# Optimization experiments

Hardware: AMD Instinct MI355X
Metric: run time of the kernel (lower is better)

Reference implementation:

```python
import jax, jax.numpy as jnp
import numpy as np

N_NODES = 100000
N_EDGES = 3200000
IN_DIM = 512
HID_DIM = 16


def spmm(edge_src, edge_dst, edge_weight, feats):
    # out[i] = sum_{(j->i) in E} w_e * feats[j]  (sparse adj @ feats)
    gathered = feats[edge_src] * edge_weight[:, None]  # [E, D]
    return jax.ops.segment_sum(gathered, edge_dst, num_segments=N_NODES)


def setup_inputs() -> dict:
    key = jax.random.key(0)
    ks = jax.random.split(key, 8)
    x = jax.random.normal(ks[0], (N_NODES, IN_DIM), dtype=jnp.float32)
    edge_src = jax.random.randint(ks[1], (N_EDGES,), 0, N_NODES, dtype=jnp.int32)
    edge_dst = jax.random.randint(ks[2], (N_EDGES,), 0, N_NODES, dtype=jnp.int32)
    # normalized adjacency weights (positive, small, like D^-1/2 A D^-1/2 entries)
    edge_weight = jax.random.uniform(ks[3], (N_EDGES,), dtype=jnp.float32) * 0.1
    # Glorot-style init for GraphConvolution weights
    W1 = jax.random.normal(ks[4], (IN_DIM, HID_DIM), dtype=jnp.float32) * (1.0 / np.sqrt(IN_DIM))
    b1 = jnp.zeros((HID_DIM,), dtype=jnp.float32)
    W2 = jax.random.normal(ks[5], (HID_DIM, 1), dtype=jnp.float32) * (1.0 / np.sqrt(HID_DIM))
    b2 = jnp.zeros((1,), dtype=jnp.float32)
    return {"x": x, "edge_src": edge_src, "edge_dst": edge_dst,
            "edge_weight": edge_weight, "W1": W1, "b1": b1, "W2": W2, "b2": b2}


def reference(x, edge_src, edge_dst, edge_weight, W1, b1, W2, b2):
    # Layer 1: GraphConvolution(input_dim -> hidden_dim) + ReLU
    h = spmm(edge_src, edge_dst, edge_weight, x @ W1) + b1  # [N, 16]
    h = jax.nn.relu(h)
    # dropout is identity in eval mode (training=False)
    # Layer 2: GraphConvolution(hidden_dim -> 1)
    out = spmm(edge_src, edge_dst, edge_weight, h @ W2) + b2  # [N, 1]
    return out
```

## Files before the change

kernel.cpp:

```cpp
#include <hip/hip_runtime.h>
#include <hip/hip_fp16.h>

#define N_NODES 100000
#define N_EDGES 3200000
#define IN_DIM  512
#define HID_DIM 16

#define B_BKT   782
#define BKT_SH  7
#define EPB     12500
#define CAP_MAX 4608

#define G1_TILES 6250

typedef __attribute__((ext_vector_type(8))) short bf16x8;
typedef __attribute__((ext_vector_type(4))) float f32x4;

__device__ __forceinline__ void atomic_add_f32(float* p, float v) {
    __hip_atomic_fetch_add(p, v, __ATOMIC_RELAXED, __HIP_MEMORY_SCOPE_AGENT);
}
__device__ __forceinline__ int atomic_add_i32(int* p, int v) {
    return __hip_atomic_fetch_add(p, v, __ATOMIC_RELAXED, __HIP_MEMORY_SCOPE_AGENT);
}

__device__ __forceinline__ unsigned short bf16_rne(float f) {
    unsigned u = __float_as_uint(f);
    return (unsigned short)((u + 0x7fffu + ((u >> 16) & 1u)) >> 16);
}

__global__ void z0_init(int* __restrict__ cursor, int cap) {
    int b = blockIdx.x * blockDim.x + threadIdx.x;
    if (b < B_BKT) cursor[b] = b * cap;
}

__global__ __launch_bounds__(256) void g1_xw_mfma(const float* __restrict__ x,
                                                  const float* __restrict__ W1,
                                                  __half* __restrict__ xwh) {
    __shared__ alignas(16) unsigned short whi[16 * 64 * 8];
    __shared__ alignas(16) unsigned short wlo[16 * 64 * 8];
    const int t = threadIdx.x;

    for (int idx = t; idx < 16 * 64 * 8; idx += 256) {
        int c  = idx >> 9;
        int l  = (idx >> 3) & 63;
        int tt = idx & 7;
        int k  = c * 32 + ((l >> 4) << 3) + tt;
        int j  = l & 15;
        float w = W1[k * HID_DIM + j];
        unsigned u = __float_as_uint(w);
        float hif = __uint_as_float(u & 0xffff0000u);
        whi[idx] = (unsigned short)(u >> 16);
        wlo[idx] = bf16_rne(w - hif);
    }
    __syncthreads();

    const int lane = t & 63;
    const int wid  = blockIdx.x * 4 + (t >> 6);
    if (wid >= G1_TILES) return;
    const int row0 = wid * 16;

    const float* xrow = x + (size_t)(row0 + (lane & 15)) * IN_DIM + ((lane >> 4) << 3);
    const unsigned short* whp = &whi[lane * 8];
    const unsigned short* wlp = &wlo[lane * 8];

    f32x4 acc = {0.f, 0.f, 0.f, 0.f};
    float4 a0 = *(const float4*)(xrow);
    float4 a1 = *(const float4*)(xrow + 4);
#pragma unroll
    for (int c = 0; c < 16; ++c) {
        float4 n0, n1;
        if (c < 15) {
            n0 = *(const float4*)(xrow + (c + 1) * 32);
            n1 = *(const float4*)(xrow + (c + 1) * 32 + 4);
        }
        float av[8] = {a0.x, a0.y, a0.z, a0.w, a1.x, a1.y, a1.z, a1.w};
        bf16x8 ah, al;
#pragma unroll
        for (int e = 0; e < 8; ++e) {
            unsigned u = __float_as_uint(av[e]);
            ah[e] = (short)(u >> 16);
            float lof = av[e] - __uint_as_float(u & 0xffff0000u);
            al[e] = (short)bf16_rne(lof);
        }
        bf16x8 bh = *(const bf16x8*)(whp + (size_t)c * 512);
        bf16x8 bl = *(const bf16x8*)(wlp + (size_t)c * 512);
        acc = __builtin_amdgcn_mfma_f32_16x16x32_bf16(ah, bh, acc, 0, 0, 0);
        acc = __builtin_amdgcn_mfma_f32_16x16x32_bf16(al, bh, acc, 0, 0, 0);
        acc = __builtin_amdgcn_mfma_f32_16x16x32_bf16(ah, bl, acc, 0, 0, 0);
        a0 = n0; a1 = n1;
    }

    const int n     = lane & 15;
    const int rbase = row0 + ((lane >> 4) << 2);
#pragma unroll
    for (int i = 0; i < 4; ++i)
        xwh[(size_t)(rbase + i) * HID_DIM + n] = __float2half_rn(acc[i]);
}

__global__ __launch_bounds__(1024) void s1_bin(const int* __restrict__ src,
                                               const int* __restrict__ dst,
                                               const float* __restrict__ wgt,
                                               int* __restrict__ cursor,
                                               uint2* __restrict__ rec, int cap) {
    __shared__ int hist[B_BKT];
    __shared__ int base[B_BKT];
    const int t = threadIdx.x;
    for (int b = t; b < B_BKT; b += 1024) hist[b] = 0;
    __syncthreads();
    const int e0 = blockIdx.x * EPB;
    const int4*   d4 = (const int4*)(dst + e0);
    const int4*   s4 = (const int4*)(src + e0);
    const float4* w4 = (const float4*)(wgt + e0);
    const int NG = EPB / 4;
    for (int g = t; g < NG; g += 1024) {
        int4 d = d4[g];
        atomicAdd(&hist[d.x >> BKT_SH], 1);
        atomicAdd(&hist[d.y >> BKT_SH], 1);
        atomicAdd(&hist[d.z >> BKT_SH], 1);
        atomicAdd(&hist[d.w >> BKT_SH], 1);
    }
    __syncthreads();
    for (int b = t; b < B_BKT; b += 1024) {
        int c = hist[b];
        base[b] = c > 0 ? atomic_add_i32(&cursor[b], c) : 0;
    }
    __syncthreads();
    for (int b = t; b < B_BKT; b += 1024) hist[b] = 0;
    __syncthreads();
    for (int g = t; g < NG; g += 1024) {
        int4 d = d4[g];
        int4 s = s4[g];
        float4 w = w4[g];
        {
            int b = d.x >> BKT_SH;
            int pos = base[b] + atomicAdd(&hist[b], 1);
            rec[pos] = make_uint2(((unsigned)s.x << BKT_SH) | (unsigned)(d.x & 127),
                                  __float_as_uint(w.x));
        }
        {
            int b = d.y >> BKT_SH;
            int pos = base[b] + atomicAdd(&hist[b], 1);
            rec[pos] = make_uint2(((unsigned)s.y << BKT_SH) | (unsigned)(d.y & 127),
                                  __float_as_uint(w.y));
        }
        {
            int b = d.z >> BKT_SH;
            int pos = base[b] + atomicAdd(&hist[b], 1);
            rec[pos] = make_uint2(((unsigned)s.z << BKT_SH) | (unsigned)(d.z & 127),
                                  __float_as_uint(w.z));
        }
        {
            int b = d.w >> BKT_SH;
            int pos = base[b] + atomicAdd(&hist[b], 1);
            rec[pos] = make_uint2(((unsigned)s.w << BKT_SH) | (unsigned)(d.w & 127),
                                  __float_as_uint(w.w));
        }
    }
}

__global__ __launch_bounds__(512) void s2_sort(const int* __restrict__ cursor,
                                               uint2* __restrict__ rec,
                                               int2* __restrict__ row, int cap) {
    __shared__ uint2 srec[CAP_MAX];
    __shared__ int ocnt[128], scn[128], cur[128];
    const int t = threadIdx.x;
    const int bkt = blockIdx.x;
    const int e0 = bkt * cap;
    int n = cursor[bkt] - e0;
    n = max(0, min(n, cap));
    if (t < 128) ocnt[t] = 0;
    __syncthreads();
    for (int i = t; i < n; i += 512) {
        uint2 r = rec[e0 + i];
        srec[i] = r;
        atomicAdd(&ocnt[r.x & 127u], 1);
    }
    __syncthreads();
    if (t < 128) scn[t] = ocnt[t];
    __syncthreads();
    for (int off = 1; off < 128; off <<= 1) {
        int v = 0;
        if (t < 128 && t >= off) v = scn[t - off];
        __syncthreads();
        if (t < 128 && t >= off) scn[t] += v;
        __syncthreads();
    }
    if (t < 128) {
        int b = scn[t] - ocnt[t];
        cur[t] = b;
        int node = (bkt << BKT_SH) + t;
        if (node < N_NODES) row[node] = make_int2(e0 + b, ocnt[t]);
    }
    __syncthreads();
    for (int i = t; i < n; i += 512) {
        uint2 r = srec[i];
        int d = (int)(r.x & 127u);
        int pos = atomicAdd(&cur[d], 1);
        rec[e0 + pos] = make_uint2(r.x >> BKT_SH, r.y);
    }
}

__global__ __launch_bounds__(256) void p4_layer1(const int2* __restrict__ row,
                                                 const uint2* __restrict__ rec,
                                                 const __half* __restrict__ xwh,
                                                 const float* __restrict__ b1,
                                                 const float* __restrict__ W2,
                                                 float* __restrict__ hw) {
    const int t = threadIdx.x;
    const int node = blockIdx.x * 16 + (t >> 4);
    const int j = t & 15;
    int2 r = row[node];
    int e = r.x;
    const int end = r.x + r.y;
    float acc = 0.0f;
    for (; e + 4 <= end; e += 4) {
        uint2 q0 = rec[e], q1 = rec[e + 1], q2 = rec[e + 2], q3 = rec[e + 3];
        float f0 = __half2float(xwh[(size_t)q0.x * HID_DIM + j]);
        float f1 = __half2float(xwh[(size_t)q1.x * HID_DIM + j]);
        float f2 = __half2float(xwh[(size_t)q2.x * HID_DIM + j]);
        float f3 = __half2float(xwh[(size_t)q3.x * HID_DIM + j]);
        acc += __uint_as_float(q0.y) * f0;
        acc += __uint_as_float(q1.y) * f1;
        acc += __uint_as_float(q2.y) * f2;
        acc += __uint_as_float(q3.y) * f3;
    }
    for (; e < end; ++e) {
        uint2 q = rec[e];
        acc += __uint_as_float(q.y) * __half2float(xwh[(size_t)q.x * HID_DIM + j]);
    }
    float v = fmaxf(acc + b1[j], 0.0f) * W2[j];
    v += __shfl_xor(v, 1);
    v += __shfl_xor(v, 2);
    v += __shfl_xor(v, 4);
    v += __shfl_xor(v, 8);
    if (j == 0) hw[node] = v;
}

__global__ __launch_bounds__(256) void p5_layer2(const int2* __restrict__ row,
                                                 const uint2* __restrict__ rec,
                                                 const float* __restrict__ hwv,
                                                 const float* __restrict__ b2,
                                                 float* __restrict__ out) {
    const int t = threadIdx.x;
    const int node = blockIdx.x * 32 + (t >> 3);
    const int i = t & 7;
    int2 r = row[node];
    const int end = r.x + r.y;
    int k = r.x + i;
    float s = 0.0f;
    for (; k + 24 < end; k += 32) {
        uint2 a = rec[k], b = rec[k + 8], c = rec[k + 16], d = rec[k + 24];
        float ha = hwv[a.x], hb = hwv[b.x], hc = hwv[c.x], hd = hwv[d.x];
        s += __uint_as_float(a.y) * ha + __uint_as_float(b.y) * hb
           + __uint_as_float(c.y) * hc + __uint_as_float(d.y) * hd;
    }
    for (; k < end; k += 8) {
        uint2 a = rec[k];
        s += __uint_as_float(a.y) * hwv[a.x];
    }
    s += __shfl_xor(s, 1);
    s += __shfl_xor(s, 2);
    s += __shfl_xor(s, 4);
    if (i == 0) out[node] = b2[0] + s;
}

__global__ void f0_zero(float* __restrict__ h, const float* __restrict__ b2,
                        float* __restrict__ out) {
    int i = blockIdx.x * blockDim.x + threadIdx.x;
    if (i < N_NODES * HID_DIM) h[i] = 0.0f;
    if (i < N_NODES) out[i] = b2[0];
}
__global__ void k2_spmm1(const int* __restrict__ src, const int* __restrict__ dst,
                         const float* __restrict__ wgt, const __half* __restrict__ xwh,
                         float* __restrict__ h) {
    int t = blockIdx.x * blockDim.x + threadIdx.x;
    int e = t >> 4;
    int j = t & (HID_DIM - 1);
    if (e < N_EDGES) {
        float v = wgt[e] * __half2float(xwh[(size_t)src[e] * HID_DIM + j]);
        atomic_add_f32(&h[(size_t)dst[e] * HID_DIM + j], v);
    }
}
__global__ void k3_act(const float* __restrict__ h, const float* __restrict__ b1,
                       const float* __restrict__ W2, float* __restrict__ hw) {
    int i = blockIdx.x * blockDim.x + threadIdx.x;
    if (i >= N_NODES) return;
    const float4* h4 = (const float4*)(h + (size_t)i * HID_DIM);
    const float4* b4 = (const float4*)b1;
    const float4* w4 = (const float4*)W2;
    float acc = 0.0f;
#pragma unroll
    for (int q = 0; q < HID_DIM / 4; ++q) {
        float4 hv = h4[q]; float4 bv = b4[q]; float4 wv = w4[q];
        acc += fmaxf(hv.x + bv.x, 0.0f) * wv.x;
        acc += fmaxf(hv.y + bv.y, 0.0f) * wv.y;
        acc += fmaxf(hv.z + bv.z, 0.0f) * wv.z;
        acc += fmaxf(hv.w + bv.w, 0.0f) * wv.w;
    }
    hw[i] = acc;
}
__global__ void k4_spmm2(const int* __restrict__ src, const int* __restrict__ dst,
                         const float* __restrict__ wgt, const float* __restrict__ hw,
                         float* __restrict__ out) {
    int e = blockIdx.x * blockDim.x + threadIdx.x;
    if (e < N_EDGES) atomic_add_f32(&out[dst[e]], wgt[e] * hw[src[e]]);
}


extern "C" void kernel_launch(void* const* d_in, const int* in_sizes, int n_in,
                              void* d_out, int out_size, void* d_ws, size_t ws_size,
                              hipStream_t stream) {
    const float* x    = (const float*)d_in[0];
    const int*   esrc = (const int*)  d_in[1];
    const int*   edst = (const int*)  d_in[2];
    const float* ew   = (const float*)d_in[3];
    const float* W1   = (const float*)d_in[4];
    const float* b1   = (const float*)d_in[5];
    const float* W2   = (const float*)d_in[6];
    const float* b2   = (const float*)d_in[7];
    float* out = (float*)d_out;
    char* ws = (char*)d_ws;

    __half* xwh    = (__half*)ws;
    float*  hw     = (float*)(ws + (size_t)N_NODES * HID_DIM * 2);
    int*    cursor = (int*)(hw + N_NODES);
    int2*   row    = (int2*)(((size_t)(cursor + B_BKT) + 7) & ~(size_t)7);
    size_t rec_off = ((size_t)((char*)(row + N_NODES) - ws) + 15) & ~(size_t)15;
    uint2* rec = (uint2*)(ws + rec_off);

    int cap = 0;
    if (ws_size > rec_off) {
        size_t cap_fit = (ws_size - rec_off) / ((size_t)B_BKT * sizeof(uint2));
        cap = (int)(cap_fit < CAP_MAX ? cap_fit : CAP_MAX);
    }

    if (cap >= 4480) {
        z0_init<<<(B_BKT + 255) / 256, 256, 0, stream>>>(cursor, cap);
        g1_xw_mfma<<<(G1_TILES + 3) / 4, 256, 0, stream>>>(x, W1, xwh);
        s1_bin<<<N_EDGES / EPB, 1024, 0, stream>>>(esrc, edst, ew, cursor, rec, cap);
        s2_sort<<<B_BKT, 512, 0, stream>>>(cursor, rec, row, cap);
        p4_layer1<<<N_NODES / 16, 256, 0, stream>>>(row, rec, xwh, b1, W2, hw);
        p5_layer2<<<N_NODES / 32, 256, 0, stream>>>(row, rec, hw, b2, out);
    } else {
        __half* f_xwh = (__half*)ws;
        float*  f_h   = (float*)(ws + (size_t)N_NODES * HID_DIM * 2);
        float*  f_hw  = f_h + (size_t)N_NODES * HID_DIM;
        int n = N_NODES * HID_DIM;
        f0_zero<<<(n + 255) / 256, 256, 0, stream>>>(f_h, b2, out);
        g1_xw_mfma<<<(G1_TILES + 3) / 4, 256, 0, stream>>>(x, W1, f_xwh);
        k2_spmm1<<<(N_EDGES * 16) / 256, 256, 0, stream>>>(esrc, edst, ew, f_xwh, f_h);
        k3_act<<<(N_NODES + 255) / 256, 256, 0, stream>>>(f_h, b1, W2, f_hw);
        k4_spmm2<<<(N_EDGES + 255) / 256, 256, 0, stream>>>(esrc, edst, ew, f_hw, out);
    }
}
```

Before: 444.9 us.

## Replace per-bucket sort with direct LDS atomic accumulation per bucket

Drops the in-bucket counting sort and the CSR row array. Both layers now process each 128-node destination bucket in one block, accumulating edge contributions with shared-memory atomics, and layer 1 applies bias, ReLU and the W2 dot product from LDS. This removes one kernel launch and the global read/write pass of the sort, at the cost of heavy LDS atomic contention. Layer 1 also runs only 782 blocks over all edges, which may limit parallelism.

```diff
diff --git a/kernel.cpp b/kernel.cpp
--- a/kernel.cpp
+++ b/kernel.cpp
@@ -158,110 +158,64 @@
     }
 }
 
-__global__ __launch_bounds__(512) void s2_sort(const int* __restrict__ cursor,
-                                               uint2* __restrict__ rec,
-                                               int2* __restrict__ row, int cap) {
-    __shared__ uint2 srec[CAP_MAX];
-    __shared__ int ocnt[128], scn[128], cur[128];
+__global__ __launch_bounds__(512) void p4_bucket(const int* __restrict__ cursor,
+                                                 const uint2* __restrict__ rec,
+                                                 const __half* __restrict__ xwh,
+                                                 const float* __restrict__ b1,
+                                                 const float* __restrict__ W2,
+                                                 float* __restrict__ hw, int cap) {
+    __shared__ float h[128 * 16];
     const int t = threadIdx.x;
     const int bkt = blockIdx.x;
     const int e0 = bkt * cap;
     int n = cursor[bkt] - e0;
     n = max(0, min(n, cap));
-    if (t < 128) ocnt[t] = 0;
-    __syncthreads();
-    for (int i = t; i < n; i += 512) {
+    for (int i = t; i < 128 * 16; i += 512) h[i] = 0.0f;
+    __syncthreads();
+    const int j = t & 15;
+    for (int i = (t >> 4); i < n; i += 32) {
         uint2 r = rec[e0 + i];
-        srec[i] = r;
-        atomicAdd(&ocnt[r.x & 127u], 1);
-    }
-    __syncthreads();
-    if (t < 128) scn[t] = ocnt[t];
-    __syncthreads();
-    for (int off = 1; off < 128; off <<= 1) {
-        int v = 0;
-        if (t < 128 && t >= off) v = scn[t - off];
-        __syncthreads();
-        if (t < 128 && t >= off) scn[t] += v;
-        __syncthreads();
-    }
+        int   d = (int)(r.x & 127u);
+        int   s = (int)(r.x >> BKT_SH);
+        float w = __uint_as_float(r.y);
+        float f = __half2float(xwh[(size_t)s * HID_DIM + j]);
+        atomicAdd(&h[(d << 4) | ((j + d) & 15)], w * f);
+    }
+    __syncthreads();
     if (t < 128) {
-        int b = scn[t] - ocnt[t];
-        cur[t] = b;
         int node = (bkt << BKT_SH) + t;
-        if (node < N_NODES) row[node] = make_int2(e0 + b, ocnt[t]);
-    }
-    __syncthreads();
-    for (int i = t; i < n; i += 512) {
-        uint2 r = srec[i];
-        int d = (int)(r.x & 127u);
-        int pos = atomicAdd(&cur[d], 1);
-        rec[e0 + pos] = make_uint2(r.x >> BKT_SH, r.y);
-    }
-}
-
-__global__ __launch_bounds__(256) void p4_layer1(const int2* __restrict__ row,
-                                                 const uint2* __restrict__ rec,
-                                                 const __half* __restrict__ xwh,
-                                                 const float* __restrict__ b1,
-                                                 const float* __restrict__ W2,
-                                                 float* __restrict__ hw) {
-    const int t = threadIdx.x;
-    const int node = blockIdx.x * 16 + (t >> 4);
-    const int j = t & 15;
-    int2 r = row[node];
-    int e = r.x;
-    const int end = r.x + r.y;
-    float acc = 0.0f;
-    for (; e + 4 <= end; e += 4) {
-        uint2 q0 = rec[e], q1 = rec[e + 1], q2 = rec[e + 2], q3 = rec[e + 3];
-        float f0 = __half2float(xwh[(size_t)q0.x * HID_DIM + j]);
-        float f1 = __half2float(xwh[(size_t)q1.x * HID_DIM + j]);
-        float f2 = __half2float(xwh[(size_t)q2.x * HID_DIM + j]);
-        float f3 = __half2float(xwh[(size_t)q3.x * HID_DIM + j]);
-        acc += __uint_as_float(q0.y) * f0;
-        acc += __uint_as_float(q1.y) * f1;
-        acc += __uint_as_float(q2.y) * f2;
-        acc += __uint_as_float(q3.y) * f3;
-    }
-    for (; e < end; ++e) {
-        uint2 q = rec[e];
-        acc += __uint_as_float(q.y) * __half2float(xwh[(size_t)q.x * HID_DIM + j]);
-    }
-    float v = fmaxf(acc + b1[j], 0.0f) * W2[j];
-    v += __shfl_xor(v, 1);
-    v += __shfl_xor(v, 2);
-    v += __shfl_xor(v, 4);
-    v += __shfl_xor(v, 8);
-    if (j == 0) hw[node] = v;
-}
-
-__global__ __launch_bounds__(256) void p5_layer2(const int2* __restrict__ row,
+        if (node < N_NODES) {
+            float v = 0.0f;
+#pragma unroll
+            for (int jj = 0; jj < 16; ++jj)
+                v += fmaxf(h[(t << 4) | ((jj + t) & 15)] + b1[jj], 0.0f) * W2[jj];
+            hw[node] = v;
+        }
+    }
+}
+
+__global__ __launch_bounds__(512) void p5_bucket(const int* __restrict__ cursor,
                                                  const uint2* __restrict__ rec,
                                                  const float* __restrict__ hwv,
                                                  const float* __restrict__ b2,
-                                                 float* __restrict__ out) {
+                                                 float* __restrict__ out, int cap) {
+    __shared__ float o[128];
     const int t = threadIdx.x;
-    const int node = blockIdx.x * 32 + (t >> 3);
-    const int i = t & 7;
-    int2 r = row[node];
-    const int end = r.x + r.y;
-    int k = r.x + i;
-    float s = 0.0f;
-    for (; k + 24 < end; k += 32) {
-        uint2 a = rec[k], b = rec[k + 8], c = rec[k + 16], d = rec[k + 24];
-        float ha = hwv[a.x], hb = hwv[b.x], hc = hwv[c.x], hd = hwv[d.x];
-        s += __uint_as_float(a.y) * ha + __uint_as_float(b.y) * hb
-           + __uint_as_float(c.y) * hc + __uint_as_float(d.y) * hd;
-    }
-    for (; k < end; k += 8) {
-        uint2 a = rec[k];
-        s += __uint_as_float(a.y) * hwv[a.x];
-    }
-    s += __shfl_xor(s, 1);
-    s += __shfl_xor(s, 2);
-    s += __shfl_xor(s, 4);
-    if (i == 0) out[node] = b2[0] + s;
+    const int bkt = blockIdx.x;
+    const int e0 = bkt * cap;
+    int n = cursor[bkt] - e0;
+    n = max(0, min(n, cap));
+    if (t < 128) o[t] = 0.0f;
+    __syncthreads();
+    for (int i = t; i < n; i += 512) {
+        uint2 r = rec[e0 + i];
+        atomicAdd(&o[r.x & 127u], __uint_as_float(r.y) * hwv[r.x >> BKT_SH]);
+    }
+    __syncthreads();
+    if (t < 128) {
+        int node = (bkt << BKT_SH) + t;
+        if (node < N_NODES) out[node] = b2[0] + o[t];
+    }
 }
 
 __global__ void f0_zero(float* __restrict__ h, const float* __restrict__ b2,
@@ -324,8 +278,7 @@
     __half* xwh    = (__half*)ws;
     float*  hw     = (float*)(ws + (size_t)N_NODES * HID_DIM * 2);
     int*    cursor = (int*)(hw + N_NODES);
-    int2*   row    = (int2*)(((size_t)(cursor + B_BKT) + 7) & ~(size_t)7);
-    size_t rec_off = ((size_t)((char*)(row + N_NODES) - ws) + 15) & ~(size_t)15;
+    size_t rec_off = ((size_t)((char*)(cursor + B_BKT) - ws) + 15) & ~(size_t)15;
     uint2* rec = (uint2*)(ws + rec_off);
 
     int cap = 0;
@@ -338,9 +291,8 @@
         z0_init<<<(B_BKT + 255) / 256, 256, 0, stream>>>(cursor, cap);
         g1_xw_mfma<<<(G1_TILES + 3) / 4, 256, 0, stream>>>(x, W1, xwh);
         s1_bin<<<N_EDGES / EPB, 1024, 0, stream>>>(esrc, edst, ew, cursor, rec, cap);
-        s2_sort<<<B_BKT, 512, 0, stream>>>(cursor, rec, row, cap);
-        p4_layer1<<<N_NODES / 16, 256, 0, stream>>>(row, rec, xwh, b1, W2, hw);
-        p5_layer2<<<N_NODES / 32, 256, 0, stream>>>(row, rec, hw, b2, out);
+        p4_bucket<<<B_BKT, 512, 0, stream>>>(cursor, rec, xwh, b1, W2, hw, cap);
+        p5_bucket<<<B_BKT, 512, 0, stream>>>(cursor, rec, hw, b2, out, cap);
     } else {
         __half* f_xwh = (__half*)ws;
         float*  f_h   = (float*)(ws + (size_t)N_NODES * HID_DIM * 2);
```

New measurement: 725.1 us. +63.0%, slower.
